# Optimization experiments

Measured on AMD Instinct MI355X. Metric: run time of the kernel, lower is better.

Reference implementation:

```python
import jax, jax.numpy as jnp
import numpy as np

# ---- model constants (match init_kwargs) ----
E = 128; GH = 8; GD = E // GH; GL = 3          # graph emb / heads / layers
SH = 4; SD = E // SH; SL = 4                   # sequence transformer
ATOM = 64; BOND = 16; RBF_K = 32; CUTOFF = 5.0
VOCAB = 64; SEQL = 128
N = 32                                          # nodes per graph (equal-size graphs)
GC = 64; GS = 16; BMOL = 16; DEG = 64; GF = 3   # conf graphs / scaffold graphs / molecules / edges-per-graph
LN_EPS = 1e-5
CENTERS = jnp.linspace(0.0, CUTOFF, RBF_K)
GAMMA = (CUTOFF / (RBF_K - 1)) ** -2            # GaussianRBF gamma = (center spacing)^-2


def _ln(x, g, b):
    mu = x.mean(-1, keepdims=True)
    var = ((x - mu) ** 2).mean(-1, keepdims=True)
    return (x - mu) / jnp.sqrt(var + LN_EPS) * g + b


def _graph_encoder(x, edge_index, edge_attr, pos, G, p):
    # node projection
    h = x @ p["gproj_w"] + p["gproj_b"]                      # [G*N, E]
    # edge features: bond features + RBF(distance)
    d = jnp.clip(edge_attr[:, -1], 0.0, 10.0)
    rbf = jnp.exp(-GAMMA * (d[:, None] - CENTERS) ** 2)       # [M, K]
    ef = jnp.concatenate([edge_attr[:, :-1], rbf], axis=1)    # [M, BOND+K]
    # EdgeNetwork: per-edge matrix (gather -> matvec -> scatter-add)
    M = ef.shape[0]
    m = (ef @ p["elin_w"] + p["elin_b"]).reshape(M, E, E)
    msg = jnp.einsum("mef,mf->me", m, h[edge_index[1]])      # [M, E]
    aggr = jnp.zeros_like(h).at[edge_index[0]].add(msg)
    h = _ln(h + aggr, p["eln_g"], p["eln_b"])
    # dense per-graph layout (equal-size graphs -> reshape, mask is all-true)
    hb = h.reshape(G, N, E)
    pp = pos.reshape(G, N, 3)
    d2 = jnp.sum((pp[:, :, None, :] - pp[:, None, :, :]) ** 2, axis=-1)
    dist = jnp.where(d2 > 0, jnp.sqrt(jnp.where(d2 > 0, d2, 1.0)), 0.0)  # safe cdist
    inv_sqrt_d = 1.0 / np.sqrt(GD)
    for l in range(GL):
        def heads(t):
            return t.reshape(G, N, GH, GD).transpose(0, 2, 1, 3)
        q = heads(hb @ p["gt_qw"][l] + p["gt_qb"][l])
        k = heads(hb @ p["gt_kw"][l] + p["gt_kb"][l])
        v = heads(hb @ p["gt_vw"][l] + p["gt_vb"][l])
        s = jnp.einsum("bhnd,bhmd->bhnm", q, k) * inv_sqrt_d + dist[:, None]
        s = jnp.clip(s, -10.0, 10.0)
        a = jax.nn.softmax(s, axis=-1)                       # all nodes valid -> no mask
        o = jnp.einsum("bhnm,bhmd->bhnd", a, v).transpose(0, 2, 1, 3).reshape(G, N, E)
        o = o @ p["gt_ow"][l] + p["gt_ob"][l]
        x1 = _ln(hb + o, p["gt_ln1g"][l], p["gt_ln1b"][l])
        ff = jax.nn.relu(x1 @ p["gt_f1w"][l] + p["gt_f1b"][l]) @ p["gt_f2w"][l] + p["gt_f2b"][l]
        hb = _ln(x1 + ff, p["gt_ln2g"][l], p["gt_ln2b"][l])
    # masked mean pool with the source's eps in the denominator
    return hb.sum(1) / (N + 1e-8)


def _seq_encoder(tokens, p):
    B, L = tokens.shape
    x = p["tok_emb"][tokens] + p["pos_emb"][:L][None]        # [B, L, E]
    inv_sqrt_d = 1.0 / np.sqrt(SD)
    for l in range(SL):
        qkv = x @ p["se_inw"][l] + p["se_inb"][l]            # [B, L, 3E]
        q, k, v = jnp.split(qkv, 3, axis=-1)
        def heads(t):
            return t.reshape(B, L, SH, SD).transpose(0, 2, 1, 3)
        q, k, v = heads(q), heads(k), heads(v)
        a = jax.nn.softmax(jnp.einsum("bhnd,bhmd->bhnm", q, k) * inv_sqrt_d, axis=-1)
        o = jnp.einsum("bhnm,bhmd->bhnd", a, v).transpose(0, 2, 1, 3).reshape(B, L, E)
        o = o @ p["se_ow"][l] + p["se_ob"][l]
        x = _ln(x + o, p["se_ln1g"][l], p["se_ln1b"][l])      # post-norm (torch default)
        ff = jax.nn.relu(x @ p["se_f1w"][l] + p["se_f1b"][l]) @ p["se_f2w"][l] + p["se_f2b"][l]
        x = _ln(x + ff, p["se_ln2g"][l], p["se_ln2b"][l])
    return x.mean(1)                                          # [B, E]


def _forward(p, conf_edge_index, scaf_edge_index, tokens, conf_per_mol):
    g_all = _graph_encoder(p["conf_x"], conf_edge_index, p["conf_edge_attr"], p["conf_pos"], GC, p)
    conf_emb = g_all.reshape(-1, conf_per_mol, E).mean(1)     # per-molecule conformer mean (equal counts)
    scaf_emb = _graph_encoder(p["scaf_x"], scaf_edge_index, p["scaf_edge_attr"], p["scaf_pos"], GS, p)
    total = conf_emb + scaf_emb
    seq = _seq_encoder(tokens, p)
    # FusionGating
    gate_h = jax.nn.relu(jnp.concatenate([total, seq], -1) @ p["fg1_w"] + p["fg1_b"])
    gate = jax.nn.sigmoid(gate_h @ p["fg2_w"] + p["fg2_b"])
    fused = gate * total + (1.0 - gate) * seq
    # CrossModalAttention: MHA over a length-1 sequence (unsqueeze(0)) -> softmax
    # weights are identically 1, so attn(q_in, kv, kv) == out_proj(v_proj(kv)).
    g, s = fused, fused
    for l in range(2):
        g2s = (s @ p["cm_g2s_vw"][l] + p["cm_g2s_vb"][l]) @ p["cm_g2s_ow"][l] + p["cm_g2s_ob"][l]
        g = _ln(g + g2s, p["cm_n1g"][l], p["cm_n1b"][l])
        s2g = (g @ p["cm_s2g_vw"][l] + p["cm_s2g_vb"][l]) @ p["cm_s2g_ow"][l] + p["cm_s2g_ob"][l]
        s = _ln(s + s2g, p["cm_n2g"][l], p["cm_n2b"][l])
    final = (g + s) * 0.5
    comb = jnp.concatenate([final, p["graph_features"]], -1)
    return (jax.nn.relu(comb @ p["r1_w"] + p["r1_b"]) @ p["r2_w"] + p["r2_b"])[:, 0]


def setup_inputs() -> dict:
    ks = iter(jax.random.split(jax.random.key(0), 64))
    def nrm(shape, s):
        return (jax.random.normal(next(ks), shape) * s).astype(jnp.float32)
    inp = {}
    def mk_graph(prefix, G):
        inp[prefix + "_x"] = nrm((G * N, ATOM), 1.0)
        off = (jnp.arange(G) * N)[:, None]
        src = jax.random.randint(next(ks), (G, DEG), 0, N) + off   # within-graph edges
        dst = jax.random.randint(next(ks), (G, DEG), 0, N) + off
        inp[prefix + "_edge_index"] = jnp.stack([src.ravel(), dst.ravel()]).astype(jnp.int32)
        bond = jax.random.uniform(next(ks), (G * DEG, BOND))
        dist = jax.random.uniform(next(ks), (G * DEG, 1), minval=0.5, maxval=CUTOFF)
        inp[prefix + "_edge_attr"] = jnp.concatenate([bond, dist], 1).astype(jnp.float32)
        inp[prefix + "_pos"] = nrm((G * N, 3), 2.0)
    mk_graph("conf", GC)
    mk_graph("scaf", GS)
    inp["tokens"] = jax.random.randint(next(ks), (BMOL, SEQL), 1, VOCAB).astype(jnp.int32)
    inp["graph_features"] = nrm((BMOL, GF), 1.0)
    inp["conf_per_mol"] = GC // BMOL
    W = 0.05
    inp["gproj_w"] = nrm((ATOM, E), W); inp["gproj_b"] = jnp.zeros(E)
    inp["elin_w"] = nrm((BOND + RBF_K, E * E), W); inp["elin_b"] = jnp.zeros(E * E)
    inp["eln_g"] = jnp.ones(E); inp["eln_b"] = jnp.zeros(E)
    for nm in ["qw", "kw", "vw", "ow"]:
        inp["gt_" + nm] = nrm((GL, E, E), W)
        inp["gt_" + nm[0] + "b"] = jnp.zeros((GL, E))
    inp["gt_ln1g"] = jnp.ones((GL, E)); inp["gt_ln1b"] = jnp.zeros((GL, E))
    inp["gt_f1w"] = nrm((GL, E, 2 * E), W); inp["gt_f1b"] = jnp.zeros((GL, 2 * E))
    inp["gt_f2w"] = nrm((GL, 2 * E, E), W); inp["gt_f2b"] = jnp.zeros((GL, E))
    inp["gt_ln2g"] = jnp.ones((GL, E)); inp["gt_ln2b"] = jnp.zeros((GL, E))
    inp["tok_emb"] = nrm((VOCAB, E), 0.02); inp["pos_emb"] = nrm((256, E), 0.02)
    inp["se_inw"] = nrm((SL, E, 3 * E), W); inp["se_inb"] = jnp.zeros((SL, 3 * E))
    inp["se_ow"] = nrm((SL, E, E), W); inp["se_ob"] = jnp.zeros((SL, E))
    inp["se_ln1g"] = jnp.ones((SL, E)); inp["se_ln1b"] = jnp.zeros((SL, E))
    inp["se_f1w"] = nrm((SL, E, 2 * E), W); inp["se_f1b"] = jnp.zeros((SL, 2 * E))
    inp["se_f2w"] = nrm((SL, 2 * E, E), W); inp["se_f2b"] = jnp.zeros((SL, E))
    inp["se_ln2g"] = jnp.ones((SL, E)); inp["se_ln2b"] = jnp.zeros((SL, E))
    inp["fg1_w"] = nrm((2 * E, 64), W); inp["fg1_b"] = jnp.zeros(64)
    inp["fg2_w"] = nrm((64, E), W); inp["fg2_b"] = jnp.zeros(E)
    for nm in ["g2s", "s2g"]:
        inp["cm_" + nm + "_vw"] = nrm((2, E, E), W); inp["cm_" + nm + "_vb"] = jnp.zeros((2, E))
        inp["cm_" + nm + "_ow"] = nrm((2, E, E), W); inp["cm_" + nm + "_ob"] = jnp.zeros((2, E))
    inp["cm_n1g"] = jnp.ones((2, E)); inp["cm_n1b"] = jnp.zeros((2, E))
    inp["cm_n2g"] = jnp.ones((2, E)); inp["cm_n2b"] = jnp.zeros((2, E))
    inp["r1_w"] = nrm((E + GF, E), W); inp["r1_b"] = jnp.zeros(E)
    inp["r2_w"] = nrm((E, 1), W); inp["r2_b"] = jnp.zeros(1)
    return inp


def reference(conf_x, conf_edge_attr, conf_pos, scaf_x, scaf_edge_attr, scaf_pos, graph_features,
              gproj_w, gproj_b, elin_w, elin_b, eln_g, eln_b,
              gt_qw, gt_qb, gt_kw, gt_kb, gt_vw, gt_vb, gt_ow, gt_ob,
              gt_ln1g, gt_ln1b, gt_f1w, gt_f1b, gt_f2w, gt_f2b, gt_ln2g, gt_ln2b,
              tok_emb, pos_emb,
              se_inw, se_inb, se_ow, se_ob, se_ln1g, se_ln1b, se_f1w, se_f1b, se_f2w, se_f2b, se_ln2g, se_ln2b,
              fg1_w, fg1_b, fg2_w, fg2_b,
              cm_g2s_vw, cm_g2s_vb, cm_g2s_ow, cm_g2s_ob, cm_n1g, cm_n1b,
              cm_s2g_vw, cm_s2g_vb, cm_s2g_ow, cm_s2g_ob, cm_n2g, cm_n2b,
              r1_w, r1_b, r2_w, r2_b,
              conf_edge_index, scaf_edge_index, tokens, conf_per_mol):
    p = dict(locals())
    return _forward(p, conf_edge_index, scaf_edge_index, tokens, conf_per_mol)
```

## Files before the change

### kernel.cpp

```cpp
#include <hip/hip_runtime.h>
#include <hip/hip_bf16.h>


__device__ __forceinline__ float blk_norm(float v, int e, float* sred)
{
  float s = v;
  #pragma unroll
  for (int o = 1; o < 64; o <<= 1) s += __shfl_xor(s, o);
  if ((e & 63) == 0) sred[e >> 6] = s;
  __syncthreads();
  float mean = (sred[0] + sred[1]) * (1.0f / 128.0f);
  __syncthreads();
  float d = v - mean;
  float s2 = d * d;
  #pragma unroll
  for (int o = 1; o < 64; o <<= 1) s2 += __shfl_xor(s2, o);
  if ((e & 63) == 0) sred[e >> 6] = s2;
  __syncthreads();
  float var = (sred[0] + sred[1]) * (1.0f / 128.0f);
  __syncthreads();
  return d / sqrtf(var + 1e-5f);
}

__global__ __launch_bounds__(128) void node_proj_k(
    const float* __restrict__ cx, const float* __restrict__ sx,
    const float* __restrict__ w, const float* __restrict__ b,
    float* __restrict__ h, float* __restrict__ aggr)
{
  int r = blockIdx.x, e = threadIdx.x;
  const float* x = (r < 2048) ? (cx + (size_t)r * 64) : (sx + (size_t)(r - 2048) * 64);
  __shared__ float xs[64];
  if (e < 64) xs[e] = x[e];
  __syncthreads();
  float acc = b[e];
  for (int a = 0; a < 64; a++) acc += xs[a] * w[a * 128 + e];
  h[(size_t)r * 128 + e] = acc;
  aggr[(size_t)r * 128 + e] = 0.0f;
}

__global__ __launch_bounds__(256) void dist_k(
    const float* __restrict__ cpos, const float* __restrict__ spos, float* __restrict__ dist)
{
  int g = blockIdx.x, tid = threadIdx.x;
  __shared__ float P[96];
  const float* p = (g < 64) ? (cpos + (size_t)g * 96) : (spos + (size_t)(g - 64) * 96);
  if (tid < 96) P[tid] = p[tid];
  __syncthreads();
  #pragma unroll
  for (int jj = 0; jj < 4; jj++) {
    int idx = tid * 4 + jj;
    int i = idx >> 5, j = idx & 31;
    float dx = P[i * 3 + 0] - P[j * 3 + 0];
    float dy = P[i * 3 + 1] - P[j * 3 + 1];
    float dz = P[i * 3 + 2] - P[j * 3 + 2];
    float d2 = dx * dx + dy * dy + dz * dz;
    dist[(size_t)g * 1024 + idx] = (d2 > 0.0f) ? sqrtf(d2) : 0.0f;
  }
}

__global__ __launch_bounds__(256) void edge_gemm_k(
    const float* __restrict__ cea, const float* __restrict__ sea,
    const int* __restrict__ cei, const int* __restrict__ sei,
    const float* __restrict__ h,
    const float* __restrict__ elw, const float* __restrict__ elb,
    float* __restrict__ aggr)
{
  __shared__ float efs[32][8];
  __shared__ float As[32][36];
  __shared__ float Bs[32][136];
  const int tid = threadIdx.x;
  const int m0 = blockIdx.x * 32;
  const int kt0 = blockIdx.y * 28;
  const int c0 = kt0 >> 2;
  {
    int t = tid >> 3, cc = tid & 7;
    if (cc < 7) {
      int c = c0 + cc;
      int m = m0 + t;
      const float* attr = (m < 4096) ? (cea + (size_t)m * 17) : (sea + (size_t)(m - 4096) * 17);
      float val;
      if (c < 16) val = attr[c];
      else if (c < 48) {
        float d = fminf(fmaxf(attr[16], 0.0f), 10.0f);
        float t2 = d - (float)((c - 16) * (5.0 / 31.0));
        val = expf(-38.44f * t2 * t2);
      } else val = 1.0f;
      efs[t][cc] = val;
    }
  }
  const int gk = tid & 31, gt = (tid >> 5) * 4;
  float hreg[4][4];
  #pragma unroll
  for (int i = 0; i < 4; i++) {
    int m = m0 + gt + i;
    int dst = (m < 4096) ? cei[4096 + m] : (sei[1024 + (m - 4096)] + 2048);
    const float* hp = h + (size_t)dst * 128 + gk;
    hreg[i][0] = hp[0]; hreg[i][1] = hp[32]; hreg[i][2] = hp[64]; hreg[i][3] = hp[96];
  }
  const int tn = tid & 31, tm = tid >> 5;
  const int e0 = 4 * tn, t0 = 4 * tm;
  const int se = tid >> 1, sk = (tid & 1) * 16;
  float acc[4][4] = {};
  __syncthreads();
  #pragma unroll 1
  for (int kt = kt0; kt < kt0 + 28; kt++) {
    int c = kt >> 2, cc = c - c0, j = kt & 3;
    float4 av;
    av.x = efs[gt + 0][cc] * hreg[0][j];
    av.y = efs[gt + 1][cc] * hreg[1][j];
    av.z = efs[gt + 2][cc] * hreg[2][j];
    av.w = efs[gt + 3][cc] * hreg[3][j];
    *(float4*)&As[gk][gt] = av;
    const float* bp = ((c < 48) ? (elw + (size_t)c * 16384) : elb) + (size_t)se * 128 + j * 32 + sk;
    float4 w0 = *(const float4*)(bp + 0);
    float4 w1 = *(const float4*)(bp + 4);
    float4 w2 = *(const float4*)(bp + 8);
    float4 w3 = *(const float4*)(bp + 12);
    Bs[sk + 0][se] = w0.x;  Bs[sk + 1][se] = w0.y;  Bs[sk + 2][se] = w0.z;  Bs[sk + 3][se] = w0.w;
    Bs[sk + 4][se] = w1.x;  Bs[sk + 5][se] = w1.y;  Bs[sk + 6][se] = w1.z;  Bs[sk + 7][se] = w1.w;
    Bs[sk + 8][se] = w2.x;  Bs[sk + 9][se] = w2.y;  Bs[sk + 10][se] = w2.z; Bs[sk + 11][se] = w2.w;
    Bs[sk + 12][se] = w3.x; Bs[sk + 13][se] = w3.y; Bs[sk + 14][se] = w3.z; Bs[sk + 15][se] = w3.w;
    __syncthreads();
    #pragma unroll
    for (int kk = 0; kk < 32; kk++) {
      float4 a = *(const float4*)&As[kk][t0];
      float4 b = *(const float4*)&Bs[kk][e0];
      acc[0][0] += a.x * b.x; acc[0][1] += a.x * b.y; acc[0][2] += a.x * b.z; acc[0][3] += a.x * b.w;
      acc[1][0] += a.y * b.x; acc[1][1] += a.y * b.y; acc[1][2] += a.y * b.z; acc[1][3] += a.y * b.w;
      acc[2][0] += a.z * b.x; acc[2][1] += a.z * b.y; acc[2][2] += a.z * b.z; acc[2][3] += a.z * b.w;
      acc[3][0] += a.w * b.x; acc[3][1] += a.w * b.y; acc[3][2] += a.w * b.z; acc[3][3] += a.w * b.w;
    }
    __syncthreads();
  }
  #pragma unroll
  for (int i = 0; i < 4; i++) {
    int m = m0 + t0 + i;
    int src = (m < 4096) ? cei[m] : (sei[m - 4096] + 2048);
    float* dst = aggr + (size_t)src * 128 + e0;
    atomicAdd(dst + 0, acc[i][0]);
    atomicAdd(dst + 1, acc[i][1]);
    atomicAdd(dst + 2, acc[i][2]);
    atomicAdd(dst + 3, acc[i][3]);
  }
}

__device__ __forceinline__ void gemm16_body(
    const float* __restrict__ A, const float* __restrict__ Bp,
    const float* __restrict__ biasp, float* __restrict__ Cp,
    int row0, int ldb, int ldc)
{
  __shared__ float Sa[32][20];
  __shared__ float Bs[32][136];
  const int tid = threadIdx.x;
  const int tm = tid >> 5, tn = tid & 31;
  const int t0 = 2 * tm, e0 = 4 * tn;
  const int ar = tid >> 4, ak = (tid & 15) * 2;
  const int bk = tid >> 3, be = (tid & 7) * 16;
  float acc[2][4] = {};
  for (int k0 = 0; k0 < 128; k0 += 32) {
    float2 av = *(const float2*)(A + (size_t)(row0 + ar) * 128 + k0 + ak);
    Sa[ak][ar] = av.x; Sa[ak + 1][ar] = av.y;
    const float* bp = Bp + (size_t)(k0 + bk) * ldb + be;
    float4 b0v = *(const float4*)(bp + 0);
    float4 b1v = *(const float4*)(bp + 4);
    float4 b2v = *(const float4*)(bp + 8);
    float4 b3v = *(const float4*)(bp + 12);
    Bs[bk][be + 0] = b0v.x;  Bs[bk][be + 1] = b0v.y;  Bs[bk][be + 2] = b0v.z;  Bs[bk][be + 3] = b0v.w;
    Bs[bk][be + 4] = b1v.x;  Bs[bk][be + 5] = b1v.y;  Bs[bk][be + 6] = b1v.z;  Bs[bk][be + 7] = b1v.w;
    Bs[bk][be + 8] = b2v.x;  Bs[bk][be + 9] = b2v.y;  Bs[bk][be + 10] = b2v.z; Bs[bk][be + 11] = b2v.w;
    Bs[bk][be + 12] = b3v.x; Bs[bk][be + 13] = b3v.y; Bs[bk][be + 14] = b3v.z; Bs[bk][be + 15] = b3v.w;
    __syncthreads();
    #pragma unroll
    for (int kk = 0; kk < 32; kk++) {
      float2 a = *(const float2*)&Sa[kk][t0];
      float4 b = *(const float4*)&Bs[kk][e0];
      acc[0][0] += a.x * b.x; acc[0][1] += a.x * b.y; acc[0][2] += a.x * b.z; acc[0][3] += a.x * b.w;
      acc[1][0] += a.y * b.x; acc[1][1] += a.y * b.y; acc[1][2] += a.y * b.z; acc[1][3] += a.y * b.w;
    }
    __syncthreads();
  }
  #pragma unroll
  for (int i = 0; i < 2; i++) {
    float* cp = Cp + (size_t)(row0 + t0 + i) * ldc + e0;
    #pragma unroll
    for (int j = 0; j < 4; j++) cp[j] = acc[i][j] + biasp[e0 + j];
  }
}

__global__ __launch_bounds__(256) void qkv_k(
    int gBlocks,
    const float* __restrict__ ghb,
    const float* gqw, const float* gkw, const float* gvw,
    const float* gqb, const float* gkb, const float* gvb, float* gout,
    const float* __restrict__ sxs, const float* sw, const float* sb, float* sout)
{
  int bx = blockIdx.x;
  if (bx < gBlocks) {
    int z = bx / 160, rt = bx % 160;
    const float* B = (z == 0) ? gqw : (z == 1) ? gkw : gvw;
    const float* bias = (z == 0) ? gqb : (z == 1) ? gkb : gvb;
    gemm16_body(ghb, B, bias, gout + (size_t)z * 327680, rt * 16, 128, 128);
  } else {
    int i = bx - gBlocks;
    int z = i >> 7, rt = i & 127;
    gemm16_body(sxs, sw + z * 128, sb + z * 128, sout + z * 128, rt * 16, 384, 384);
  }
}

__device__ __forceinline__ void gattn_body(
    int g, int h, const float* __restrict__ q, const float* __restrict__ k,
    const float* __restrict__ v, const float* __restrict__ dist, float* __restrict__ o)
{
  __shared__ float qs[32][17], ksh[32][17], vsh[32][17], ss[32][33], rs[32];
  const int tid = threadIdx.x;
  {
    int idx = tid * 2;
    int i = idx >> 4, d = idx & 15;
    size_t base = ((size_t)(g * 32 + i)) * 128 + h * 16 + d;
    qs[i][d] = q[base];  qs[i][d + 1] = q[base + 1];
    ksh[i][d] = k[base]; ksh[i][d + 1] = k[base + 1];
    vsh[i][d] = v[base]; vsh[i][d + 1] = v[base + 1];
  }
  __syncthreads();
  {
    int i = tid >> 3, j0 = (tid & 7) * 4;
    for (int j = j0; j < j0 + 4; j++) {
      float a = 0;
      #pragma unroll
      for (int d = 0; d < 16; d++) a += qs[i][d] * ksh[j][d];
      a = a * 0.25f + dist[(size_t)g * 1024 + i * 32 + j];
      ss[i][j] = fminf(fmaxf(a, -10.0f), 10.0f);
    }
  }
  __syncthreads();
  if (tid < 32) {
    float m = -1e30f;
    for (int j = 0; j < 32; j++) m = fmaxf(m, ss[tid][j]);
    float sm = 0;
    for (int j = 0; j < 32; j++) { float ex = expf(ss[tid][j] - m); ss[tid][j] = ex; sm += ex; }
    rs[tid] = 1.0f / sm;
  }
  __syncthreads();
  {
    int idx = tid * 2;
    int i = idx >> 4, d = idx & 15;
    float a0 = 0, a1 = 0;
    for (int j = 0; j < 32; j++) { float wj = ss[i][j]; a0 += wj * vsh[j][d]; a1 += wj * vsh[j][d + 1]; }
    float r = rs[i];
    size_t base = ((size_t)(g * 32 + i)) * 128 + h * 16 + d;
    o[base] = a0 * r; o[base + 1] = a1 * r;
  }
}

__device__ __forceinline__ void sattn_body(
    int b, int h, int qt, const float* __restrict__ qkv, float* __restrict__ o)
{
  __shared__ float ks[128][33];
  __shared__ float vs[128][33];
  __shared__ float qs2[32][33];
  __shared__ float ss2[32][129];
  __shared__ float red[32][8];
  __shared__ float red2[32][8];
  const int tid = threadIdx.x;
  {
    int l = tid >> 1, d0 = (tid & 1) * 16;
    const float* kp = qkv + ((size_t)(b * 128 + l)) * 384 + 128 + h * 32 + d0;
    #pragma unroll
    for (int j = 0; j < 16; j++) { ks[l][d0 + j] = kp[j]; vs[l][d0 + j] = kp[128 + j]; }
  }
  {
    int i = tid >> 3, d0 = (tid & 7) * 4;
    const float* qp = qkv + ((size_t)(b * 128 + qt * 32 + i)) * 384 + h * 32 + d0;
    #pragma unroll
    for (int j = 0; j < 4; j++) qs2[i][d0 + j] = qp[j];
  }
  __syncthreads();
  const int i = tid >> 3, sub = tid & 7;
  {
    int j0 = sub * 16;
    for (int j = j0; j < j0 + 16; j++) {
      float a = 0;
      #pragma unroll
      for (int d = 0; d < 32; d++) a += qs2[i][d] * ks[j][d];
      ss2[i][j] = a * 0.17677669529663687f;
    }
  }
  __syncthreads();
  float m = -1e30f;
  for (int j = sub; j < 128; j += 8) m = fmaxf(m, ss2[i][j]);
  red[i][sub] = m;
  __syncthreads();
  float mm = red[i][0];
  #pragma unroll
  for (int t = 1; t < 8; t++) mm = fmaxf(mm, red[i][t]);
  float ps = 0;
  for (int j = sub; j < 128; j += 8) { float ex = expf(ss2[i][j] - mm); ss2[i][j] = ex; ps += ex; }
  red2[i][sub] = ps;
  __syncthreads();
  float sm = 0;
  #pragma unroll
  for (int t = 0; t < 8; t++) sm += red2[i][t];
  float rinv = 1.0f / sm;
  {
    int d0 = sub * 4;
    float a0 = 0, a1 = 0, a2 = 0, a3 = 0;
    for (int j = 0; j < 128; j++) {
      float wj = ss2[i][j];
      a0 += wj * vs[j][d0 + 0]; a1 += wj * vs[j][d0 + 1];
      a2 += wj * vs[j][d0 + 2]; a3 += wj * vs[j][d0 + 3];
    }
    float* op = o + ((size_t)(b * 128 + qt * 32 + i)) * 128 + h * 32 + d0;
    op[0] = a0 * rinv; op[1] = a1 * rinv; op[2] = a2 * rinv; op[3] = a3 * rinv;
  }
}

__global__ __launch_bounds__(256) void attn_k(
    int gBlocks, const float* q, const float* k, const float* v,
    const float* dist, float* go, const float* qkv, float* so)
{
  int bx = blockIdx.x;
  if (bx < gBlocks) gattn_body(bx >> 3, bx & 7, q, k, v, dist, go);
  else { int i = bx - gBlocks; sattn_body(i >> 4, (i >> 2) & 3, i & 3, qkv, so); }
}

__device__ __forceinline__ void tail_body(
    int row0, const float* __restrict__ A,
    const float* __restrict__ Wo, const float* __restrict__ bo, const float* __restrict__ res,
    const float* __restrict__ g1, const float* __restrict__ b1n,
    const float* __restrict__ W1, const float* __restrict__ b1f,
    const float* __restrict__ W2, const float* __restrict__ b2f,
    const float* __restrict__ g2, const float* __restrict__ b2n,
    float* __restrict__ Out)
{
  __shared__ float x1[16][132];
  __shared__ float hid[16][260];
  __shared__ __align__(16) float sbuf[4352];
  __shared__ float Sa[32][20];
  float (*BsA)[136] = (float(*)[136])sbuf;
  float (*Bs1)[260] = (float(*)[260])sbuf;
  float (*Bs2)[136] = (float(*)[136])sbuf;
  const int tid = threadIdx.x;
  {
    const int tm = tid >> 5, tn = tid & 31;
    const int t0 = 2 * tm, e0 = 4 * tn;
    const int ar = tid >> 4, ak = (tid & 15) * 2;
    const int bk = tid >> 3, be = (tid & 7) * 16;
    float acc[2][4] = {};
    for (int k0 = 0; k0 < 128; k0 += 32) {
      float2 av = *(const float2*)(A + (size_t)(row0 + ar) * 128 + k0 + ak);
      Sa[ak][ar] = av.x; Sa[ak + 1][ar] = av.y;
      const float* bp = Wo + (size_t)(k0 + bk) * 128 + be;
      float4 b0v = *(const float4*)(bp + 0);
      float4 b1v = *(const float4*)(bp + 4);
      float4 b2v = *(const float4*)(bp + 8);
      float4 b3v = *(const float4*)(bp + 12);
      BsA[bk][be + 0] = b0v.x;  BsA[bk][be + 1] = b0v.y;  BsA[bk][be + 2] = b0v.z;  BsA[bk][be + 3] = b0v.w;
      BsA[bk][be + 4] = b1v.x;  BsA[bk][be + 5] = b1v.y;  BsA[bk][be + 6] = b1v.z;  BsA[bk][be + 7] = b1v.w;
      BsA[bk][be + 8] = b2v.x;  BsA[bk][be + 9] = b2v.y;  BsA[bk][be + 10] = b2v.z; BsA[bk][be + 11] = b2v.w;
      BsA[bk][be + 12] = b3v.x; BsA[bk][be + 13] = b3v.y; BsA[bk][be + 14] = b3v.z; BsA[bk][be + 15] = b3v.w;
      __syncthreads();
      #pragma unroll
      for (int kk = 0; kk < 32; kk++) {
        float2 a = *(const float2*)&Sa[kk][t0];
        float4 b = *(const float4*)&BsA[kk][e0];
        acc[0][0] += a.x * b.x; acc[0][1] += a.x * b.y; acc[0][2] += a.x * b.z; acc[0][3] += a.x * b.w;
        acc[1][0] += a.y * b.x; acc[1][1] += a.y * b.y; acc[1][2] += a.y * b.z; acc[1][3] += a.y * b.w;
      }
      __syncthreads();
    }
    #pragma unroll
    for (int i = 0; i < 2; i++) {
      int r = row0 + t0 + i;
      float v0 = acc[i][0] + bo[e0 + 0] + res[(size_t)r * 128 + e0 + 0];
      float v1 = acc[i][1] + bo[e0 + 1] + res[(size_t)r * 128 + e0 + 1];
      float v2 = acc[i][2] + bo[e0 + 2] + res[(size_t)r * 128 + e0 + 2];
      float v3 = acc[i][3] + bo[e0 + 3] + res[(size_t)r * 128 + e0 + 3];
      float s = v0 + v1 + v2 + v3;
      #pragma unroll
      for (int o = 1; o < 32; o <<= 1) s += __shfl_xor(s, o);
      float mean = s * (1.0f / 128.0f);
      float d0 = v0 - mean, d1 = v1 - mean, d2 = v2 - mean, d3 = v3 - mean;
      float sq = d0 * d0 + d1 * d1 + d2 * d2 + d3 * d3;
      #pragma unroll
      for (int o = 1; o < 32; o <<= 1) sq += __shfl_xor(sq, o);
      float rstd = 1.0f / sqrtf(sq * (1.0f / 128.0f) + 1e-5f);
      x1[t0 + i][e0 + 0] = d0 * rstd * g1[e0 + 0] + b1n[e0 + 0];
      x1[t0 + i][e0 + 1] = d1 * rstd * g1[e0 + 1] + b1n[e0 + 1];
      x1[t0 + i][e0 + 2] = d2 * rstd * g1[e0 + 2] + b1n[e0 + 2];
      x1[t0 + i][e0 + 3] = d3 * rstd * g1[e0 + 3] + b1n[e0 + 3];
    }
  }
  __syncthreads();
  {
    const int tm = tid >> 6, tn = tid & 63;
    const int t0 = 4 * tm, e0 = 4 * tn;
    const int ar = tid >> 4, ak = tid & 15;
    const int bk = tid >> 4, be = (tid & 15) * 16;
    float acc[4][4] = {};
    for (int k0 = 0; k0 < 128; k0 += 16) {
      Sa[ak][ar] = x1[ar][k0 + ak];
      const float* bp = W1 + (size_t)(k0 + bk) * 256 + be;
      float4 b0v = *(const float4*)(bp + 0);
      float4 b1v = *(const float4*)(bp + 4);
      float4 b2v = *(const float4*)(bp + 8);
      float4 b3v = *(const float4*)(bp + 12);
      Bs1[bk][be + 0] = b0v.x;  Bs1[bk][be + 1] = b0v.y;  Bs1[bk][be + 2] = b0v.z;  Bs1[bk][be + 3] = b0v.w;
      Bs1[bk][be + 4] = b1v.x;  Bs1[bk][be + 5] = b1v.y;  Bs1[bk][be + 6] = b1v.z;  Bs1[bk][be + 7] = b1v.w;
      Bs1[bk][be + 8] = b2v.x;  Bs1[bk][be + 9] = b2v.y;  Bs1[bk][be + 10] = b2v.z; Bs1[bk][be + 11] = b2v.w;
      Bs1[bk][be + 12] = b3v.x; Bs1[bk][be + 13] = b3v.y; Bs1[bk][be + 14] = b3v.z; Bs1[bk][be + 15] = b3v.w;
      __syncthreads();
      #pragma unroll
      for (int kk = 0; kk < 16; kk++) {
        float4 a = *(const float4*)&Sa[kk][t0];
        float4 b = *(const float4*)&Bs1[kk][e0];
        acc[0][0] += a.x * b.x; acc[0][1] += a.x * b.y; acc[0][2] += a.x * b.z; acc[0][3] += a.x * b.w;
        acc[1][0] += a.y * b.x; acc[1][1] += a.y * b.y; acc[1][2] += a.y * b.z; acc[1][3] += a.y * b.w;
        acc[2][0] += a.z * b.x; acc[2][1] += a.z * b.y; acc[2][2] += a.z * b.z; acc[2][3] += a.z * b.w;
        acc[3][0] += a.w * b.x; acc[3][1] += a.w * b.y; acc[3][2] += a.w * b.z; acc[3][3] += a.w * b.w;
      }
      __syncthreads();
    }
    #pragma unroll
    for (int i = 0; i < 4; i++) {
      float4 hv;
      hv.x = fmaxf(acc[i][0] + b1f[e0 + 0], 0.0f);
      hv.y = fmaxf(acc[i][1] + b1f[e0 + 1], 0.0f);
      hv.z = fmaxf(acc[i][2] + b1f[e0 + 2], 0.0f);
      hv.w = fmaxf(acc[i][3] + b1f[e0 + 3], 0.0f);
      *(float4*)&hid[t0 + i][e0] = hv;
    }
  }
  __syncthreads();
  {
    const int tm = tid >> 5, tn = tid & 31;
    const int t0 = 2 * tm, e0 = 4 * tn;
    const int bk = tid >> 3, be = (tid & 7) * 16;
    float acc[2][4] = {};
    for (int k0 = 0; k0 < 256; k0 += 32) {
      const float* bp = W2 + (size_t)(k0 + bk) * 128 + be;
      float4 b0v = *(const float4*)(bp + 0);
      float4 b1v = *(const float4*)(bp + 4);
      float4 b2v = *(const float4*)(bp + 8);
      float4 b3v = *(const float4*)(bp + 12);
      Bs2[bk][be + 0] = b0v.x;  Bs2[bk][be + 1] = b0v.y;  Bs2[bk][be + 2] = b0v.z;  Bs2[bk][be + 3] = b0v.w;
      Bs2[bk][be + 4] = b1v.x;  Bs2[bk][be + 5] = b1v.y;  Bs2[bk][be + 6] = b1v.z;  Bs2[bk][be + 7] = b1v.w;
      Bs2[bk][be + 8] = b2v.x;  Bs2[bk][be + 9] = b2v.y;  Bs2[bk][be + 10] = b2v.z; Bs2[bk][be + 11] = b2v.w;
      Bs2[bk][be + 12] = b3v.x; Bs2[bk][be + 13] = b3v.y; Bs2[bk][be + 14] = b3v.z; Bs2[bk][be + 15] = b3v.w;
      __syncthreads();
      #pragma unroll
      for (int kk = 0; kk < 32; kk++) {
        float a0 = hid[t0 + 0][k0 + kk];
        float a1 = hid[t0 + 1][k0 + kk];
        float4 b = *(const float4*)&Bs2[kk][e0];
        acc[0][0] += a0 * b.x; acc[0][1] += a0 * b.y; acc[0][2] += a0 * b.z; acc[0][3] += a0 * b.w;
        acc[1][0] += a1 * b.x; acc[1][1] += a1 * b.y; acc[1][2] += a1 * b.z; acc[1][3] += a1 * b.w;
      }
      __syncthreads();
    }
    #pragma unroll
    for (int i = 0; i < 2; i++) {
      int r = row0 + t0 + i;
      float v0 = acc[i][0] + b2f[e0 + 0] + x1[t0 + i][e0 + 0];
      float v1 = acc[i][1] + b2f[e0 + 1] + x1[t0 + i][e0 + 1];
      float v2 = acc[i][2] + b2f[e0 + 2] + x1[t0 + i][e0 + 2];
      float v3 = acc[i][3] + b2f[e0 + 3] + x1[t0 + i][e0 + 3];
      float s = v0 + v1 + v2 + v3;
      #pragma unroll
      for (int o = 1; o < 32; o <<= 1) s += __shfl_xor(s, o);
      float mean = s * (1.0f / 128.0f);
      float d0 = v0 - mean, d1 = v1 - mean, d2 = v2 - mean, d3 = v3 - mean;
      float sq = d0 * d0 + d1 * d1 + d2 * d2 + d3 * d3;
      #pragma unroll
      for (int o = 1; o < 32; o <<= 1) sq += __shfl_xor(sq, o);
      float rstd = 1.0f / sqrtf(sq * (1.0f / 128.0f) + 1e-5f);
      float* cp = Out + (size_t)r * 128 + e0;
      cp[0] = d0 * rstd * g2[e0 + 0] + b2n[e0 + 0];
      cp[1] = d1 * rstd * g2[e0 + 1] + b2n[e0 + 1];
      cp[2] = d2 * rstd * g2[e0 + 2] + b2n[e0 + 2];
      cp[3] = d3 * rstd * g2[e0 + 3] + b2n[e0 + 3];
    }
  }
}

__global__ __launch_bounds__(256) void tail_k(
    int gBlocks,
    const float* gA, const float* gWo, const float* gbo, const float* gres,
    const float* gg1, const float* gb1, const float* gW1, const float* gbf1,
    const float* gW2, const float* gbf2, const float* gg2, const float* gb2, float* gOut,
    const float* sA, const float* sWo, const float* sbo, const float* sres,
    const float* sg1, const float* sb1, const float* sW1, const float* sbf1,
    const float* sW2, const float* sbf2, const float* sg2, const float* sb2, float* sOut)
{
  int bx = blockIdx.x;
  if (bx < gBlocks)
    tail_body(bx * 16, gA, gWo, gbo, gres, gg1, gb1, gW1, gbf1, gW2, gbf2, gg2, gb2, gOut);
  else
    tail_body((bx - gBlocks) * 16, sA, sWo, sbo, sres, sg1, sb1, sW1, sbf1, sW2, sbf2, sg2, sb2, sOut);
}

__global__ __launch_bounds__(128) void ln_k(
    const float* __restrict__ x, const float* __restrict__ res,
    const float* __restrict__ g, const float* __restrict__ b, float* __restrict__ out)
{
  __shared__ float sred[2];
  int r = blockIdx.x, e = threadIdx.x;
  size_t idx = (size_t)r * 128 + e;
  float v = x[idx] + res[idx];
  float nv = blk_norm(v, e, sred);
  out[idx] = nv * g[e] + b[e];
}

__global__ __launch_bounds__(128) void embed_k(
    const int* __restrict__ tokens, const float* __restrict__ tok_emb,
    const float* __restrict__ pos_emb, float* __restrict__ xs)
{
  int r = blockIdx.x, e = threadIdx.x;
  int tk = tokens[r];
  xs[(size_t)r * 128 + e] = tok_emb[(size_t)tk * 128 + e] + pos_emb[(size_t)(r & 127) * 128 + e];
}

__global__ __launch_bounds__(128) void head_k(
    const float* __restrict__ hb, const float* __restrict__ xs, const float* __restrict__ gfeat,
    const float* fg1w, const float* fg1b, const float* fg2w, const float* fg2b,
    const float* g2s_vw, const float* g2s_vb, const float* g2s_ow, const float* g2s_ob,
    const float* n1g, const float* n1b,
    const float* s2g_vw, const float* s2g_vb, const float* s2g_ow, const float* s2g_ob,
    const float* n2g, const float* n2b,
    const float* r1w, const float* r1b, const float* r2w, const float* r2b,
    float* __restrict__ out)
{
  __shared__ float T[128], S[128], G[128], Sm[128], t1[128], t2[128], gh[64], sred[2];
  int mol = blockIdx.x, e = threadIdx.x;
  {
    float cs = 0;
    for (int c = 0; c < 4; c++) {
      int g = mol * 4 + c;
      float s = 0;
      for (int i = 0; i < 32; i++) s += hb[((size_t)(g * 32 + i)) * 128 + e];
      cs += s * (1.0f / 32.0f);
    }
    cs *= 0.25f;
    float s2 = 0;
    int g = 64 + mol;
    for (int i = 0; i < 32; i++) s2 += hb[((size_t)(g * 32 + i)) * 128 + e];
    T[e] = cs + s2 * (1.0f / 32.0f);
    float ss = 0;
    for (int l = 0; l < 128; l++) ss += xs[((size_t)(mol * 128 + l)) * 128 + e];
    S[e] = ss * (1.0f / 128.0f);
  }
  __syncthreads();
  if (e < 64) {
    float a = fg1b[e];
    for (int f = 0; f < 128; f++) a += T[f] * fg1w[f * 64 + e];
    for (int f = 0; f < 128; f++) a += S[f] * fg1w[(128 + f) * 64 + e];
    gh[e] = fmaxf(a, 0.0f);
  }
  __syncthreads();
  {
    float a = fg2b[e];
    for (int j = 0; j < 64; j++) a += gh[j] * fg2w[j * 128 + e];
    float gate = 1.0f / (1.0f + expf(-a));
    float fu = gate * T[e] + (1.0f - gate) * S[e];
    G[e] = fu; Sm[e] = fu;
  }
  __syncthreads();
  for (int l = 0; l < 2; l++) {
    const float* vw = g2s_vw + (size_t)l * 16384; const float* vb = g2s_vb + l * 128;
    const float* ow = g2s_ow + (size_t)l * 16384; const float* ob = g2s_ob + l * 128;
    float a = vb[e];
    for (int f = 0; f < 128; f++) a += Sm[f] * vw[f * 128 + e];
    t1[e] = a;
    __syncthreads();
    a = ob[e];
    for (int f = 0; f < 128; f++) a += t1[f] * ow[f * 128 + e];
    float nv = blk_norm(G[e] + a, e, sred);
    G[e] = nv * n1g[l * 128 + e] + n1b[l * 128 + e];
    __syncthreads();
    const float* vw2 = s2g_vw + (size_t)l * 16384; const float* vb2 = s2g_vb + l * 128;
    const float* ow2 = s2g_ow + (size_t)l * 16384; const float* ob2 = s2g_ob + l * 128;
    a = vb2[e];
    for (int f = 0; f < 128; f++) a += G[f] * vw2[f * 128 + e];
    t1[e] = a;
    __syncthreads();
    a = ob2[e];
    for (int f = 0; f < 128; f++) a += t1[f] * ow2[f * 128 + e];
    nv = blk_norm(Sm[e] + a, e, sred);
    Sm[e] = nv * n2g[l * 128 + e] + n2b[l * 128 + e];
    __syncthreads();
  }
  t2[e] = 0.5f * (G[e] + Sm[e]);
  __syncthreads();
  float a = r1b[e];
  for (int f = 0; f < 128; f++) a += t2[f] * r1w[f * 128 + e];
  for (int f = 0; f < 3; f++) a += gfeat[mol * 3 + f] * r1w[(128 + f) * 128 + e];
  a = fmaxf(a, 0.0f);
  float p = a * r2w[e];
  #pragma unroll
  for (int o = 1; o < 64; o <<= 1) p += __shfl_xor(p, o);
  if ((e & 63) == 0) sred[e >> 6] = p;
  __syncthreads();
  if (e == 0) out[mol] = sred[0] + sred[1] + r2b[0];
}

extern "C" void kernel_launch(void* const* d_in, const int* in_sizes, int n_in,
                              void* d_out, int out_size, void* d_ws, size_t ws_size,
                              hipStream_t stream)
{
  (void)n_in; (void)out_size; (void)ws_size;
  const bool dict = (in_sizes[1] == 8192);
  auto IN = [&](int di, int si) { return d_in[dict ? di : si]; };

  const float* conf_x   = (const float*)IN(0, 0);
  const int*   conf_ei  = (const int*)  IN(1, 63);
  const float* conf_ea  = (const float*)IN(2, 1);
  const float* conf_pos = (const float*)IN(3, 2);
  const float* scaf_x   = (const float*)IN(4, 3);
  const int*   scaf_ei  = (const int*)  IN(5, 64);
  const float* scaf_ea  = (const float*)IN(6, 4);
  const float* scaf_pos = (const float*)IN(7, 5);
  const int*   tokens   = (const int*)  IN(8, 65);
  const float* gfeat    = (const float*)IN(9, 6);
  const float* gproj_w  = (const float*)IN(11, 7);
  const float* gproj_b  = (const float*)IN(12, 8);
  const float* elin_w   = (const float*)IN(13, 9);
  const float* elin_b   = (const float*)IN(14, 10);
  const float* eln_g    = (const float*)IN(15, 11);
  const float* eln_b    = (const float*)IN(16, 12);
  const float* gt_qw    = (const float*)IN(17, 13);
  const float* gt_qb    = (const float*)IN(18, 14);
  const float* gt_kw    = (const float*)IN(19, 15);
  const float* gt_kb    = (const float*)IN(20, 16);
  const float* gt_vw    = (const float*)IN(21, 17);
  const float* gt_vb    = (const float*)IN(22, 18);
  const float* gt_ow    = (const float*)IN(23, 19);
  const float* gt_ob    = (const float*)IN(24, 20);
  const float* gt_ln1g  = (const float*)IN(25, 21);
  const float* gt_ln1b  = (const float*)IN(26, 22);
  const float* gt_f1w   = (const float*)IN(27, 23);
  const float* gt_f1b   = (const float*)IN(28, 24);
  const float* gt_f2w   = (const float*)IN(29, 25);
  const float* gt_f2b   = (const float*)IN(30, 26);
  const float* gt_ln2g  = (const float*)IN(31, 27);
  const float* gt_ln2b  = (const float*)IN(32, 28);
  const float* tok_emb  = (const float*)IN(33, 29);
  const float* pos_emb  = (const float*)IN(34, 30);
  const float* se_inw   = (const float*)IN(35, 31);
  const float* se_inb   = (const float*)IN(36, 32);
  const float* se_ow    = (const float*)IN(37, 33);
  const float* se_ob    = (const float*)IN(38, 34);
  const float* se_ln1g  = (const float*)IN(39, 35);
  const float* se_ln1b  = (const float*)IN(40, 36);
  const float* se_f1w   = (const float*)IN(41, 37);
  const float* se_f1b   = (const float*)IN(42, 38);
  const float* se_f2w   = (const float*)IN(43, 39);
  const float* se_f2b   = (const float*)IN(44, 40);
  const float* se_ln2g  = (const float*)IN(45, 41);
  const float* se_ln2b  = (const float*)IN(46, 42);
  const float* fg1_w    = (const float*)IN(47, 43);
  const float* fg1_b    = (const float*)IN(48, 44);
  const float* fg2_w    = (const float*)IN(49, 45);
  const float* fg2_b    = (const float*)IN(50, 46);
  const float* cm_g2s_vw = (const float*)IN(51, 47);
  const float* cm_g2s_vb = (const float*)IN(52, 48);
  const float* cm_g2s_ow = (const float*)IN(53, 49);
  const float* cm_g2s_ob = (const float*)IN(54, 50);
  const float* cm_s2g_vw = (const float*)IN(55, 53);
  const float* cm_s2g_vb = (const float*)IN(56, 54);
  const float* cm_s2g_ow = (const float*)IN(57, 55);
  const float* cm_s2g_ob = (const float*)IN(58, 56);
  const float* cm_n1g   = (const float*)IN(59, 51);
  const float* cm_n1b   = (const float*)IN(60, 52);
  const float* cm_n2g   = (const float*)IN(61, 57);
  const float* cm_n2b   = (const float*)IN(62, 58);
  const float* r1_w     = (const float*)IN(63, 59);
  const float* r1_b     = (const float*)IN(64, 60);
  const float* r2_w     = (const float*)IN(65, 61);
  const float* r2_b     = (const float*)IN(66, 62);
  float* out = (float*)d_out;

  float* w = (float*)d_ws;
  size_t off = 0;
  auto alloc = [&](size_t n) { float* p = w + off; off += n; return p; };
  float* h     = alloc(2560 * 128);
  float* aggr  = alloc(2560 * 128);
  float* hb    = alloc(2560 * 128);
  float* distb = alloc(80 * 1024);
  float* qb    = alloc(3 * 327680);
  float* atto  = alloc(327680);
  float* xs2   = alloc(2048 * 128);
  float* qkv3  = alloc(2048 * 384);
  float* satto = alloc(2048 * 128);
  float* xsfin = alloc(2048 * 128);

  node_proj_k<<<2560, 128, 0, stream>>>(conf_x, scaf_x, gproj_w, gproj_b, h, aggr);
  dist_k<<<80, 256, 0, stream>>>(conf_pos, scaf_pos, distb);
  edge_gemm_k<<<dim3(160, 7), 256, 0, stream>>>(conf_ea, scaf_ea, conf_ei, scaf_ei, h, elin_w, elin_b, aggr);
  ln_k<<<2560, 128, 0, stream>>>(aggr, h, eln_g, eln_b, hb);
  embed_k<<<2048, 128, 0, stream>>>(tokens, tok_emb, pos_emb, xs2);

  for (int l = 0; l < 4; l++) {
    const bool hasG = (l < 3);
    const int lg = hasG ? l : 0;
    const int gq = hasG ? 480 : 0;
    const int ga = hasG ? 640 : 0;
    const int gt = hasG ? 160 : 0;
    float* sOut = (l == 3) ? xsfin : xs2;
    qkv_k<<<gq + 384, 256, 0, stream>>>(gq,
        hb, gt_qw + (size_t)lg * 16384, gt_kw + (size_t)lg * 16384, gt_vw + (size_t)lg * 16384,
        gt_qb + lg * 128, gt_kb + lg * 128, gt_vb + lg * 128, qb,
        xs2, se_inw + (size_t)l * 49152, se_inb + l * 384, qkv3);
    attn_k<<<ga + 256, 256, 0, stream>>>(ga, qb, qb + 327680, qb + 655360, distb, atto, qkv3, satto);
    tail_k<<<gt + 128, 256, 0, stream>>>(gt,
        atto, gt_ow + (size_t)lg * 16384, gt_ob + lg * 128, hb,
        gt_ln1g + lg * 128, gt_ln1b + lg * 128,
        gt_f1w + (size_t)lg * 32768, gt_f1b + lg * 256,
        gt_f2w + (size_t)lg * 32768, gt_f2b + lg * 128,
        gt_ln2g + lg * 128, gt_ln2b + lg * 128, hb,
        satto, se_ow + (size_t)l * 16384, se_ob + l * 128, xs2,
        se_ln1g + l * 128, se_ln1b + l * 128,
        se_f1w + (size_t)l * 32768, se_f1b + l * 256,
        se_f2w + (size_t)l * 32768, se_f2b + l * 128,
        se_ln2g + l * 128, se_ln2b + l * 128, sOut);
  }

  head_k<<<16, 128, 0, stream>>>(hb, xsfin, gfeat,
                                 fg1_w, fg1_b, fg2_w, fg2_b,
                                 cm_g2s_vw, cm_g2s_vb, cm_g2s_ow, cm_g2s_ob, cm_n1g, cm_n1b,
                                 cm_s2g_vw, cm_s2g_vb, cm_s2g_ow, cm_s2g_ob, cm_n2g, cm_n2b,
                                 r1_w, r1_b, r2_w, r2_b, out);
}
```

Before: 663.6 us.

## Fuse front kernels and restructure small GEMMs to stage A in LDS

Node projection, distance and embedding kernels are merged into one launch to cut launch overhead. The QKV and tail GEMMs now stage the whole 16x128 A tile in shared memory and read B directly from global memory per column, dropping the K-tiled B staging and most barriers. Sequence attention streams K and V in 32-row chunks through a shared buffer, and shared memory is unioned to cut LDS footprint and raise occupancy. The cost is uncached-in-LDS global reads of the weights per block and more barriers in attention.

```diff
diff --git a/kernel.cpp b/kernel.cpp
--- a/kernel.cpp
+++ b/kernel.cpp
@@ -22,39 +22,45 @@
   return d / sqrtf(var + 1e-5f);
 }
 
-__global__ __launch_bounds__(128) void node_proj_k(
+__global__ __launch_bounds__(256) void front_k(
     const float* __restrict__ cx, const float* __restrict__ sx,
     const float* __restrict__ w, const float* __restrict__ b,
-    float* __restrict__ h, float* __restrict__ aggr)
-{
-  int r = blockIdx.x, e = threadIdx.x;
-  const float* x = (r < 2048) ? (cx + (size_t)r * 64) : (sx + (size_t)(r - 2048) * 64);
-  __shared__ float xs[64];
-  if (e < 64) xs[e] = x[e];
-  __syncthreads();
-  float acc = b[e];
-  for (int a = 0; a < 64; a++) acc += xs[a] * w[a * 128 + e];
-  h[(size_t)r * 128 + e] = acc;
-  aggr[(size_t)r * 128 + e] = 0.0f;
-}
-
-__global__ __launch_bounds__(256) void dist_k(
-    const float* __restrict__ cpos, const float* __restrict__ spos, float* __restrict__ dist)
-{
-  int g = blockIdx.x, tid = threadIdx.x;
-  __shared__ float P[96];
-  const float* p = (g < 64) ? (cpos + (size_t)g * 96) : (spos + (size_t)(g - 64) * 96);
-  if (tid < 96) P[tid] = p[tid];
-  __syncthreads();
-  #pragma unroll
-  for (int jj = 0; jj < 4; jj++) {
-    int idx = tid * 4 + jj;
-    int i = idx >> 5, j = idx & 31;
-    float dx = P[i * 3 + 0] - P[j * 3 + 0];
-    float dy = P[i * 3 + 1] - P[j * 3 + 1];
-    float dz = P[i * 3 + 2] - P[j * 3 + 2];
-    float d2 = dx * dx + dy * dy + dz * dz;
-    dist[(size_t)g * 1024 + idx] = (d2 > 0.0f) ? sqrtf(d2) : 0.0f;
+    float* __restrict__ h, float* __restrict__ aggr,
+    const float* __restrict__ cpos, const float* __restrict__ spos, float* __restrict__ dist,
+    const int* __restrict__ tokens, const float* __restrict__ tok_emb,
+    const float* __restrict__ pos_emb, float* __restrict__ xs)
+{
+  __shared__ float sP[128];
+  const int bx = blockIdx.x, tid = threadIdx.x;
+  if (bx < 1280) {
+    int r = bx * 2 + (tid >> 7), e = tid & 127;
+    const float* x = (r < 2048) ? (cx + (size_t)r * 64) : (sx + (size_t)(r - 2048) * 64);
+    float* xrow = sP + (tid >> 7) * 64;
+    if (e < 64) xrow[e] = x[e];
+    __syncthreads();
+    float acc = b[e];
+    for (int a = 0; a < 64; a++) acc += xrow[a] * w[a * 128 + e];
+    h[(size_t)r * 128 + e] = acc;
+    aggr[(size_t)r * 128 + e] = 0.0f;
+  } else if (bx < 1360) {
+    int g = bx - 1280;
+    const float* p = (g < 64) ? (cpos + (size_t)g * 96) : (spos + (size_t)(g - 64) * 96);
+    if (tid < 96) sP[tid] = p[tid];
+    __syncthreads();
+    #pragma unroll
+    for (int jj = 0; jj < 4; jj++) {
+      int idx = tid * 4 + jj;
+      int i = idx >> 5, j = idx & 31;
+      float dx = sP[i * 3 + 0] - sP[j * 3 + 0];
+      float dy = sP[i * 3 + 1] - sP[j * 3 + 1];
+      float dz = sP[i * 3 + 2] - sP[j * 3 + 2];
+      float d2 = dx * dx + dy * dy + dz * dz;
+      dist[(size_t)g * 1024 + idx] = (d2 > 0.0f) ? sqrtf(d2) : 0.0f;
+    }
+  } else {
+    int r = (bx - 1360) * 2 + (tid >> 7), e = tid & 127;
+    int tk = tokens[r];
+    xs[(size_t)r * 128 + e] = tok_emb[(size_t)tk * 128 + e] + pos_emb[(size_t)(r & 127) * 128 + e];
   }
 }
 
@@ -144,47 +150,36 @@
   }
 }
 
-__device__ __forceinline__ void gemm16_body(
+__device__ __forceinline__ void sgemm16_body(float (*Al)[132],
     const float* __restrict__ A, const float* __restrict__ Bp,
     const float* __restrict__ biasp, float* __restrict__ Cp,
     int row0, int ldb, int ldc)
 {
-  __shared__ float Sa[32][20];
-  __shared__ float Bs[32][136];
   const int tid = threadIdx.x;
-  const int tm = tid >> 5, tn = tid & 31;
-  const int t0 = 2 * tm, e0 = 4 * tn;
-  const int ar = tid >> 4, ak = (tid & 15) * 2;
-  const int bk = tid >> 3, be = (tid & 7) * 16;
-  float acc[2][4] = {};
-  for (int k0 = 0; k0 < 128; k0 += 32) {
-    float2 av = *(const float2*)(A + (size_t)(row0 + ar) * 128 + k0 + ak);
-    Sa[ak][ar] = av.x; Sa[ak + 1][ar] = av.y;
-    const float* bp = Bp + (size_t)(k0 + bk) * ldb + be;
-    float4 b0v = *(const float4*)(bp + 0);
-    float4 b1v = *(const float4*)(bp + 4);
-    float4 b2v = *(const float4*)(bp + 8);
-    float4 b3v = *(const float4*)(bp + 12);
-    Bs[bk][be + 0] = b0v.x;  Bs[bk][be + 1] = b0v.y;  Bs[bk][be + 2] = b0v.z;  Bs[bk][be + 3] = b0v.w;
-    Bs[bk][be + 4] = b1v.x;  Bs[bk][be + 5] = b1v.y;  Bs[bk][be + 6] = b1v.z;  Bs[bk][be + 7] = b1v.w;
-    Bs[bk][be + 8] = b2v.x;  Bs[bk][be + 9] = b2v.y;  Bs[bk][be + 10] = b2v.z; Bs[bk][be + 11] = b2v.w;
-    Bs[bk][be + 12] = b3v.x; Bs[bk][be + 13] = b3v.y; Bs[bk][be + 14] = b3v.z; Bs[bk][be + 15] = b3v.w;
-    __syncthreads();
-    #pragma unroll
-    for (int kk = 0; kk < 32; kk++) {
-      float2 a = *(const float2*)&Sa[kk][t0];
-      float4 b = *(const float4*)&Bs[kk][e0];
-      acc[0][0] += a.x * b.x; acc[0][1] += a.x * b.y; acc[0][2] += a.x * b.z; acc[0][3] += a.x * b.w;
-      acc[1][0] += a.y * b.x; acc[1][1] += a.y * b.y; acc[1][2] += a.y * b.z; acc[1][3] += a.y * b.w;
-    }
-    __syncthreads();
-  }
-  #pragma unroll
-  for (int i = 0; i < 2; i++) {
-    float* cp = Cp + (size_t)(row0 + t0 + i) * ldc + e0;
-    #pragma unroll
-    for (int j = 0; j < 4; j++) cp[j] = acc[i][j] + biasp[e0 + j];
-  }
+  const int c = tid & 127, rg = tid >> 7;
+  for (int i = tid; i < 512; i += 256) {
+    int r = i >> 5, k4 = (i & 31) << 2;
+    *(float4*)&Al[r][k4] = *(const float4*)(A + (size_t)(row0 + r) * 128 + k4);
+  }
+  __syncthreads();
+  float acc[8] = {};
+  const float* bp = Bp + c;
+  #pragma unroll 4
+  for (int k = 0; k < 128; k += 4) {
+    float b0 = bp[(size_t)(k + 0) * ldb];
+    float b1 = bp[(size_t)(k + 1) * ldb];
+    float b2 = bp[(size_t)(k + 2) * ldb];
+    float b3 = bp[(size_t)(k + 3) * ldb];
+    #pragma unroll
+    for (int i = 0; i < 8; i++) {
+      float4 a = *(const float4*)&Al[rg * 8 + i][k];
+      acc[i] += a.x * b0; acc[i] += a.y * b1; acc[i] += a.z * b2; acc[i] += a.w * b3;
+    }
+  }
+  float bia = biasp[c];
+  #pragma unroll
+  for (int i = 0; i < 8; i++)
+    Cp[(size_t)(row0 + rg * 8 + i) * ldc + c] = acc[i] + bia;
 }
 
 __global__ __launch_bounds__(256) void qkv_k(
@@ -194,32 +189,33 @@
     const float* gqb, const float* gkb, const float* gvb, float* gout,
     const float* __restrict__ sxs, const float* sw, const float* sb, float* sout)
 {
+  __shared__ float Al[16][132];
   int bx = blockIdx.x;
   if (bx < gBlocks) {
     int z = bx / 160, rt = bx % 160;
     const float* B = (z == 0) ? gqw : (z == 1) ? gkw : gvw;
     const float* bias = (z == 0) ? gqb : (z == 1) ? gkb : gvb;
-    gemm16_body(ghb, B, bias, gout + (size_t)z * 327680, rt * 16, 128, 128);
+    sgemm16_body(Al, ghb, B, bias, gout + (size_t)z * 327680, rt * 16, 128, 128);
   } else {
     int i = bx - gBlocks;
     int z = i >> 7, rt = i & 127;
-    gemm16_body(sxs, sw + z * 128, sb + z * 128, sout + z * 128, rt * 16, 384, 384);
-  }
-}
-
-__device__ __forceinline__ void gattn_body(
-    int g, int h, const float* __restrict__ q, const float* __restrict__ k,
+    sgemm16_body(Al, sxs, sw + z * 128, sb + z * 128, sout + z * 128, rt * 16, 384, 384);
+  }
+}
+
+struct __align__(16) GAttnSm { float qs[32][17], ksh[32][17], vsh[32][17], ss[32][33], rs[32]; };
+__device__ __forceinline__ void gattn_body(GAttnSm& sm, int g, int h,
+    const float* __restrict__ q, const float* __restrict__ k,
     const float* __restrict__ v, const float* __restrict__ dist, float* __restrict__ o)
 {
-  __shared__ float qs[32][17], ksh[32][17], vsh[32][17], ss[32][33], rs[32];
   const int tid = threadIdx.x;
   {
     int idx = tid * 2;
     int i = idx >> 4, d = idx & 15;
     size_t base = ((size_t)(g * 32 + i)) * 128 + h * 16 + d;
-    qs[i][d] = q[base];  qs[i][d + 1] = q[base + 1];
-    ksh[i][d] = k[base]; ksh[i][d + 1] = k[base + 1];
-    vsh[i][d] = v[base]; vsh[i][d + 1] = v[base + 1];
+    sm.qs[i][d] = q[base];  sm.qs[i][d + 1] = q[base + 1];
+    sm.ksh[i][d] = k[base]; sm.ksh[i][d + 1] = k[base + 1];
+    sm.vsh[i][d] = v[base]; sm.vsh[i][d + 1] = v[base + 1];
   }
   __syncthreads();
   {
@@ -227,104 +223,114 @@
     for (int j = j0; j < j0 + 4; j++) {
       float a = 0;
       #pragma unroll
-      for (int d = 0; d < 16; d++) a += qs[i][d] * ksh[j][d];
+      for (int d = 0; d < 16; d++) a += sm.qs[i][d] * sm.ksh[j][d];
       a = a * 0.25f + dist[(size_t)g * 1024 + i * 32 + j];
-      ss[i][j] = fminf(fmaxf(a, -10.0f), 10.0f);
+      sm.ss[i][j] = fminf(fmaxf(a, -10.0f), 10.0f);
     }
   }
   __syncthreads();
   if (tid < 32) {
     float m = -1e30f;
-    for (int j = 0; j < 32; j++) m = fmaxf(m, ss[tid][j]);
-    float sm = 0;
-    for (int j = 0; j < 32; j++) { float ex = expf(ss[tid][j] - m); ss[tid][j] = ex; sm += ex; }
-    rs[tid] = 1.0f / sm;
+    for (int j = 0; j < 32; j++) m = fmaxf(m, sm.ss[tid][j]);
+    float s = 0;
+    for (int j = 0; j < 32; j++) { float ex = expf(sm.ss[tid][j] - m); sm.ss[tid][j] = ex; s += ex; }
+    sm.rs[tid] = 1.0f / s;
   }
   __syncthreads();
   {
     int idx = tid * 2;
     int i = idx >> 4, d = idx & 15;
     float a0 = 0, a1 = 0;
-    for (int j = 0; j < 32; j++) { float wj = ss[i][j]; a0 += wj * vsh[j][d]; a1 += wj * vsh[j][d + 1]; }
-    float r = rs[i];
+    for (int j = 0; j < 32; j++) { float wj = sm.ss[i][j]; a0 += wj * sm.vsh[j][d]; a1 += wj * sm.vsh[j][d + 1]; }
+    float r = sm.rs[i];
     size_t base = ((size_t)(g * 32 + i)) * 128 + h * 16 + d;
     o[base] = a0 * r; o[base + 1] = a1 * r;
   }
 }
 
-__device__ __forceinline__ void sattn_body(
-    int b, int h, int qt, const float* __restrict__ qkv, float* __restrict__ o)
-{
-  __shared__ float ks[128][33];
-  __shared__ float vs[128][33];
-  __shared__ float qs2[32][33];
-  __shared__ float ss2[32][129];
-  __shared__ float red[32][8];
-  __shared__ float red2[32][8];
+struct __align__(16) SAttnSm { float kv[32][33], qs2[32][33], ss2[32][129], red[32][8], red2[32][8]; };
+__device__ __forceinline__ void sattn_body(SAttnSm& sm, int b, int h, int qt,
+    const float* __restrict__ qkv, float* __restrict__ o)
+{
   const int tid = threadIdx.x;
-  {
-    int l = tid >> 1, d0 = (tid & 1) * 16;
-    const float* kp = qkv + ((size_t)(b * 128 + l)) * 384 + 128 + h * 32 + d0;
-    #pragma unroll
-    for (int j = 0; j < 16; j++) { ks[l][d0 + j] = kp[j]; vs[l][d0 + j] = kp[128 + j]; }
-  }
   {
     int i = tid >> 3, d0 = (tid & 7) * 4;
     const float* qp = qkv + ((size_t)(b * 128 + qt * 32 + i)) * 384 + h * 32 + d0;
-    #pragma unroll
-    for (int j = 0; j < 4; j++) qs2[i][d0 + j] = qp[j];
-  }
-  __syncthreads();
+    sm.qs2[i][d0 + 0] = qp[0]; sm.qs2[i][d0 + 1] = qp[1];
+    sm.qs2[i][d0 + 2] = qp[2]; sm.qs2[i][d0 + 3] = qp[3];
+  }
   const int i = tid >> 3, sub = tid & 7;
-  {
-    int j0 = sub * 16;
-    for (int j = j0; j < j0 + 16; j++) {
-      float a = 0;
-      #pragma unroll
-      for (int d = 0; d < 32; d++) a += qs2[i][d] * ks[j][d];
-      ss2[i][j] = a * 0.17677669529663687f;
-    }
-  }
-  __syncthreads();
+  for (int jt = 0; jt < 4; jt++) {
+    {
+      int r = tid >> 3, dd = (tid & 7) * 4;
+      const float* kp = qkv + ((size_t)(b * 128 + jt * 32 + r)) * 384 + 128 + h * 32 + dd;
+      float4 kv4 = *(const float4*)kp;
+      sm.kv[r][dd + 0] = kv4.x; sm.kv[r][dd + 1] = kv4.y;
+      sm.kv[r][dd + 2] = kv4.z; sm.kv[r][dd + 3] = kv4.w;
+    }
+    __syncthreads();
+    {
+      int j0 = jt * 32 + sub * 4;
+      for (int j = j0; j < j0 + 4; j++) {
+        int jr = j - jt * 32;
+        float a = 0;
+        #pragma unroll
+        for (int d = 0; d < 32; d++) a += sm.qs2[i][d] * sm.kv[jr][d];
+        sm.ss2[i][j] = a * 0.17677669529663687f;
+      }
+    }
+    __syncthreads();
+  }
   float m = -1e30f;
-  for (int j = sub; j < 128; j += 8) m = fmaxf(m, ss2[i][j]);
-  red[i][sub] = m;
-  __syncthreads();
-  float mm = red[i][0];
-  #pragma unroll
-  for (int t = 1; t < 8; t++) mm = fmaxf(mm, red[i][t]);
+  for (int j = sub; j < 128; j += 8) m = fmaxf(m, sm.ss2[i][j]);
+  sm.red[i][sub] = m;
+  __syncthreads();
+  float mm = sm.red[i][0];
+  #pragma unroll
+  for (int t = 1; t < 8; t++) mm = fmaxf(mm, sm.red[i][t]);
   float ps = 0;
-  for (int j = sub; j < 128; j += 8) { float ex = expf(ss2[i][j] - mm); ss2[i][j] = ex; ps += ex; }
-  red2[i][sub] = ps;
-  __syncthreads();
-  float sm = 0;
-  #pragma unroll
-  for (int t = 0; t < 8; t++) sm += red2[i][t];
-  float rinv = 1.0f / sm;
-  {
-    int d0 = sub * 4;
-    float a0 = 0, a1 = 0, a2 = 0, a3 = 0;
-    for (int j = 0; j < 128; j++) {
-      float wj = ss2[i][j];
-      a0 += wj * vs[j][d0 + 0]; a1 += wj * vs[j][d0 + 1];
-      a2 += wj * vs[j][d0 + 2]; a3 += wj * vs[j][d0 + 3];
-    }
-    float* op = o + ((size_t)(b * 128 + qt * 32 + i)) * 128 + h * 32 + d0;
-    op[0] = a0 * rinv; op[1] = a1 * rinv; op[2] = a2 * rinv; op[3] = a3 * rinv;
-  }
-}
-
+  for (int j = sub; j < 128; j += 8) { float ex = expf(sm.ss2[i][j] - mm); sm.ss2[i][j] = ex; ps += ex; }
+  sm.red2[i][sub] = ps;
+  __syncthreads();
+  float s = 0;
+  #pragma unroll
+  for (int t = 0; t < 8; t++) s += sm.red2[i][t];
+  float rinv = 1.0f / s;
+  float a0 = 0, a1 = 0, a2 = 0, a3 = 0;
+  const int d0 = sub * 4;
+  for (int jt = 0; jt < 4; jt++) {
+    __syncthreads();
+    {
+      int r = tid >> 3, dd = (tid & 7) * 4;
+      const float* vp = qkv + ((size_t)(b * 128 + jt * 32 + r)) * 384 + 256 + h * 32 + dd;
+      float4 vv = *(const float4*)vp;
+      sm.kv[r][dd + 0] = vv.x; sm.kv[r][dd + 1] = vv.y;
+      sm.kv[r][dd + 2] = vv.z; sm.kv[r][dd + 3] = vv.w;
+    }
+    __syncthreads();
+    for (int jr = 0; jr < 32; jr++) {
+      float wj = sm.ss2[i][jt * 32 + jr];
+      a0 += wj * sm.kv[jr][d0 + 0]; a1 += wj * sm.kv[jr][d0 + 1];
+      a2 += wj * sm.kv[jr][d0 + 2]; a3 += wj * sm.kv[jr][d0 + 3];
+    }
+  }
+  float* op = o + ((size_t)(b * 128 + qt * 32 + i)) * 128 + h * 32 + d0;
+  op[0] = a0 * rinv; op[1] = a1 * rinv; op[2] = a2 * rinv; op[3] = a3 * rinv;
+}
+
+union AttnU { GAttnSm a; SAttnSm s; };
 __global__ __launch_bounds__(256) void attn_k(
     int gBlocks, const float* q, const float* k, const float* v,
     const float* dist, float* go, const float* qkv, float* so)
 {
+  __shared__ AttnU u;
   int bx = blockIdx.x;
-  if (bx < gBlocks) gattn_body(bx >> 3, bx & 7, q, k, v, dist, go);
-  else { int i = bx - gBlocks; sattn_body(i >> 4, (i >> 2) & 3, i & 3, qkv, so); }
-}
-
-__device__ __forceinline__ void tail_body(
-    int row0, const float* __restrict__ A,
+  if (bx < gBlocks) gattn_body(u.a, bx >> 3, bx & 7, q, k, v, dist, go);
+  else { int i = bx - gBlocks; sattn_body(u.s, i >> 4, (i >> 2) & 3, i & 3, qkv, so); }
+}
+
+struct __align__(16) TailSm2 { float x1v[16][132]; float big[16][260]; };
+__device__ __forceinline__ void tail_body(TailSm2& sm, int row0, const float* __restrict__ A,
     const float* __restrict__ Wo, const float* __restrict__ bo, const float* __restrict__ res,
     const float* __restrict__ g1, const float* __restrict__ b1n,
     const float* __restrict__ W1, const float* __restrict__ b1f,
@@ -332,49 +338,42 @@
     const float* __restrict__ g2, const float* __restrict__ b2n,
     float* __restrict__ Out)
 {
-  __shared__ float x1[16][132];
-  __shared__ float hid[16][260];
-  __shared__ __align__(16) float sbuf[4352];
-  __shared__ float Sa[32][20];
-  float (*BsA)[136] = (float(*)[136])sbuf;
-  float (*Bs1)[260] = (float(*)[260])sbuf;
-  float (*Bs2)[136] = (float(*)[136])sbuf;
   const int tid = threadIdx.x;
+  const int c = tid & 127, rg = tid >> 7;
+  for (int i = tid; i < 512; i += 256) {
+    int r = i >> 5, k4 = (i & 31) << 2;
+    *(float4*)&sm.big[r][k4] = *(const float4*)(A + (size_t)(row0 + r) * 128 + k4);
+  }
+  __syncthreads();
+  {
+    float acc[8] = {};
+    const float* bp = Wo + c;
+    #pragma unroll 4
+    for (int k = 0; k < 128; k += 4) {
+      float b0 = bp[(k + 0) * 128], b1 = bp[(k + 1) * 128];
+      float b2 = bp[(k + 2) * 128], b3 = bp[(k + 3) * 128];
+      #pragma unroll
+      for (int i = 0; i < 8; i++) {
+        float4 a = *(const float4*)&sm.big[rg * 8 + i][k];
+        acc[i] += a.x * b0; acc[i] += a.y * b1; acc[i] += a.z * b2; acc[i] += a.w * b3;
+      }
+    }
+    float bia = bo[c];
+    #pragma unroll
+    for (int i = 0; i < 8; i++) {
+      int r = rg * 8 + i;
+      sm.x1v[r][c] = acc[i] + bia + res[(size_t)(row0 + r) * 128 + c];
+    }
+  }
+  __syncthreads();
   {
     const int tm = tid >> 5, tn = tid & 31;
     const int t0 = 2 * tm, e0 = 4 * tn;
-    const int ar = tid >> 4, ak = (tid & 15) * 2;
-    const int bk = tid >> 3, be = (tid & 7) * 16;
-    float acc[2][4] = {};
-    for (int k0 = 0; k0 < 128; k0 += 32) {
-      float2 av = *(const float2*)(A + (size_t)(row0 + ar) * 128 + k0 + ak);
-      Sa[ak][ar] = av.x; Sa[ak + 1][ar] = av.y;
-      const float* bp = Wo + (size_t)(k0 + bk) * 128 + be;
-      float4 b0v = *(const float4*)(bp + 0);
-      float4 b1v = *(const float4*)(bp + 4);
-      float4 b2v = *(const float4*)(bp + 8);
-      float4 b3v = *(const float4*)(bp + 12);
-      BsA[bk][be + 0] = b0v.x;  BsA[bk][be + 1] = b0v.y;  BsA[bk][be + 2] = b0v.z;  BsA[bk][be + 3] = b0v.w;
-      BsA[bk][be + 4] = b1v.x;  BsA[bk][be + 5] = b1v.y;  BsA[bk][be + 6] = b1v.z;  BsA[bk][be + 7] = b1v.w;
-      BsA[bk][be + 8] = b2v.x;  BsA[bk][be + 9] = b2v.y;  BsA[bk][be + 10] = b2v.z; BsA[bk][be + 11] = b2v.w;
-      BsA[bk][be + 12] = b3v.x; BsA[bk][be + 13] = b3v.y; BsA[bk][be + 14] = b3v.z; BsA[bk][be + 15] = b3v.w;
-      __syncthreads();
-      #pragma unroll
-      for (int kk = 0; kk < 32; kk++) {
-        float2 a = *(const float2*)&Sa[kk][t0];
-        float4 b = *(const float4*)&BsA[kk][e0];
-        acc[0][0] += a.x * b.x; acc[0][1] += a.x * b.y; acc[0][2] += a.x * b.z; acc[0][3] += a.x * b.w;
-        acc[1][0] += a.y * b.x; acc[1][1] += a.y * b.y; acc[1][2] += a.y * b.z; acc[1][3] += a.y * b.w;
-      }
-      __syncthreads();
-    }
     #pragma unroll
     for (int i = 0; i < 2; i++) {
-      int r = row0 + t0 + i;
-      float v0 = acc[i][0] + bo[e0 + 0] + res[(size_t)r * 128 + e0 + 0];
-      float v1 = acc[i][1] + bo[e0 + 1] + res[(size_t)r * 128 + e0 + 1];
-      float v2 = acc[i][2] + bo[e0 + 2] + res[(size_t)r * 128 + e0 + 2];
-      float v3 = acc[i][3] + bo[e0 + 3] + res[(size_t)r * 128 + e0 + 3];
+      int r = t0 + i;
+      float v0 = sm.x1v[r][e0 + 0], v1 = sm.x1v[r][e0 + 1];
+      float v2 = sm.x1v[r][e0 + 2], v3 = sm.x1v[r][e0 + 3];
       float s = v0 + v1 + v2 + v3;
       #pragma unroll
       for (int o = 1; o < 32; o <<= 1) s += __shfl_xor(s, o);
@@ -384,86 +383,63 @@
       #pragma unroll
       for (int o = 1; o < 32; o <<= 1) sq += __shfl_xor(sq, o);
       float rstd = 1.0f / sqrtf(sq * (1.0f / 128.0f) + 1e-5f);
-      x1[t0 + i][e0 + 0] = d0 * rstd * g1[e0 + 0] + b1n[e0 + 0];
-      x1[t0 + i][e0 + 1] = d1 * rstd * g1[e0 + 1] + b1n[e0 + 1];
-      x1[t0 + i][e0 + 2] = d2 * rstd * g1[e0 + 2] + b1n[e0 + 2];
-      x1[t0 + i][e0 + 3] = d3 * rstd * g1[e0 + 3] + b1n[e0 + 3];
-    }
-  }
-  __syncthreads();
-  {
-    const int tm = tid >> 6, tn = tid & 63;
-    const int t0 = 4 * tm, e0 = 4 * tn;
-    const int ar = tid >> 4, ak = tid & 15;
-    const int bk = tid >> 4, be = (tid & 15) * 16;
-    float acc[4][4] = {};
-    for (int k0 = 0; k0 < 128; k0 += 16) {
-      Sa[ak][ar] = x1[ar][k0 + ak];
-      const float* bp = W1 + (size_t)(k0 + bk) * 256 + be;
-      float4 b0v = *(const float4*)(bp + 0);
-      float4 b1v = *(const float4*)(bp + 4);
-      float4 b2v = *(const float4*)(bp + 8);
-      float4 b3v = *(const float4*)(bp + 12);
-      Bs1[bk][be + 0] = b0v.x;  Bs1[bk][be + 1] = b0v.y;  Bs1[bk][be + 2] = b0v.z;  Bs1[bk][be + 3] = b0v.w;
-      Bs1[bk][be + 4] = b1v.x;  Bs1[bk][be + 5] = b1v.y;  Bs1[bk][be + 6] = b1v.z;  Bs1[bk][be + 7] = b1v.w;
-      Bs1[bk][be + 8] = b2v.x;  Bs1[bk][be + 9] = b2v.y;  Bs1[bk][be + 10] = b2v.z; Bs1[bk][be + 11] = b2v.w;
-      Bs1[bk][be + 12] = b3v.x; Bs1[bk][be + 13] = b3v.y; Bs1[bk][be + 14] = b3v.z; Bs1[bk][be + 15] = b3v.w;
-      __syncthreads();
-      #pragma unroll
-      for (int kk = 0; kk < 16; kk++) {
-        float4 a = *(const float4*)&Sa[kk][t0];
-        float4 b = *(const float4*)&Bs1[kk][e0];
-        acc[0][0] += a.x * b.x; acc[0][1] += a.x * b.y; acc[0][2] += a.x * b.z; acc[0][3] += a.x * b.w;
-        acc[1][0] += a.y * b.x; acc[1][1] += a.y * b.y; acc[1][2] += a.y * b.z; acc[1][3] += a.y * b.w;
-        acc[2][0] += a.z * b.x; acc[2][1] += a.z * b.y; acc[2][2] += a.z * b.z; acc[2][3] += a.z * b.w;
-        acc[3][0] += a.w * b.x; acc[3][1] += a.w * b.y; acc[3][2] += a.w * b.z; acc[3][3] += a.w * b.w;
+      sm.x1v[r][e0 + 0] = d0 * rstd * g1[e0 + 0] + b1n[e0 + 0];
+      sm.x1v[r][e0 + 1] = d1 * rstd * g1[e0 + 1] + b1n[e0 + 1];
+      sm.x1v[r][e0 + 2] = d2 * rstd * g1[e0 + 2] + b1n[e0 + 2];
+      sm.x1v[r][e0 + 3] = d3 * rstd * g1[e0 + 3] + b1n[e0 + 3];
+    }
+  }
+  __syncthreads();
+  {
+    float acc[16] = {};
+    const float* bp = W1 + tid;
+    #pragma unroll 2
+    for (int k = 0; k < 128; k += 4) {
+      float b0 = bp[(k + 0) * 256], b1 = bp[(k + 1) * 256];
+      float b2 = bp[(k + 2) * 256], b3 = bp[(k + 3) * 256];
+      #pragma unroll
+      for (int i = 0; i < 16; i++) {
+        float4 a = *(const float4*)&sm.x1v[i][k];
+        acc[i] += a.x * b0; acc[i] += a.y * b1; acc[i] += a.z * b2; acc[i] += a.w * b3;
       }
-      __syncthreads();
-    }
-    #pragma unroll
-    for (int i = 0; i < 4; i++) {
-      float4 hv;
-      hv.x = fmaxf(acc[i][0] + b1f[e0 + 0], 0.0f);
-      hv.y = fmaxf(acc[i][1] + b1f[e0 + 1], 0.0f);
-      hv.z = fmaxf(acc[i][2] + b1f[e0 + 2], 0.0f);
-      hv.w = fmaxf(acc[i][3] + b1f[e0 + 3], 0.0f);
-      *(float4*)&hid[t0 + i][e0] = hv;
-    }
+    }
+    float bia = b1f[tid];
+    __syncthreads();
+    #pragma unroll
+    for (int i = 0; i < 16; i++)
+      sm.big[i][tid] = fmaxf(acc[i] + bia, 0.0f);
+  }
+  __syncthreads();
+  {
+    float acc[8] = {};
+    const float* bp = W2 + c;
+    #pragma unroll 4
+    for (int k = 0; k < 256; k += 4) {
+      float b0 = bp[(k + 0) * 128], b1 = bp[(k + 1) * 128];
+      float b2 = bp[(k + 2) * 128], b3 = bp[(k + 3) * 128];
+      #pragma unroll
+      for (int i = 0; i < 8; i++) {
+        float4 a = *(const float4*)&sm.big[rg * 8 + i][k];
+        acc[i] += a.x * b0; acc[i] += a.y * b1; acc[i] += a.z * b2; acc[i] += a.w * b3;
+      }
+    }
+    float bia = b2f[c];
+    float v[8];
+    #pragma unroll
+    for (int i = 0; i < 8; i++) v[i] = acc[i] + bia + sm.x1v[rg * 8 + i][c];
+    __syncthreads();
+    #pragma unroll
+    for (int i = 0; i < 8; i++) sm.x1v[rg * 8 + i][c] = v[i];
   }
   __syncthreads();
   {
     const int tm = tid >> 5, tn = tid & 31;
     const int t0 = 2 * tm, e0 = 4 * tn;
-    const int bk = tid >> 3, be = (tid & 7) * 16;
-    float acc[2][4] = {};
-    for (int k0 = 0; k0 < 256; k0 += 32) {
-      const float* bp = W2 + (size_t)(k0 + bk) * 128 + be;
-      float4 b0v = *(const float4*)(bp + 0);
-      float4 b1v = *(const float4*)(bp + 4);
-      float4 b2v = *(const float4*)(bp + 8);
-      float4 b3v = *(const float4*)(bp + 12);
-      Bs2[bk][be + 0] = b0v.x;  Bs2[bk][be + 1] = b0v.y;  Bs2[bk][be + 2] = b0v.z;  Bs2[bk][be + 3] = b0v.w;
-      Bs2[bk][be + 4] = b1v.x;  Bs2[bk][be + 5] = b1v.y;  Bs2[bk][be + 6] = b1v.z;  Bs2[bk][be + 7] = b1v.w;
-      Bs2[bk][be + 8] = b2v.x;  Bs2[bk][be + 9] = b2v.y;  Bs2[bk][be + 10] = b2v.z; Bs2[bk][be + 11] = b2v.w;
-      Bs2[bk][be + 12] = b3v.x; Bs2[bk][be + 13] = b3v.y; Bs2[bk][be + 14] = b3v.z; Bs2[bk][be + 15] = b3v.w;
-      __syncthreads();
-      #pragma unroll
-      for (int kk = 0; kk < 32; kk++) {
-        float a0 = hid[t0 + 0][k0 + kk];
-        float a1 = hid[t0 + 1][k0 + kk];
-        float4 b = *(const float4*)&Bs2[kk][e0];
-        acc[0][0] += a0 * b.x; acc[0][1] += a0 * b.y; acc[0][2] += a0 * b.z; acc[0][3] += a0 * b.w;
-        acc[1][0] += a1 * b.x; acc[1][1] += a1 * b.y; acc[1][2] += a1 * b.z; acc[1][3] += a1 * b.w;
-      }
-      __syncthreads();
-    }
     #pragma unroll
     for (int i = 0; i < 2; i++) {
-      int r = row0 + t0 + i;
-      float v0 = acc[i][0] + b2f[e0 + 0] + x1[t0 + i][e0 + 0];
-      float v1 = acc[i][1] + b2f[e0 + 1] + x1[t0 + i][e0 + 1];
-      float v2 = acc[i][2] + b2f[e0 + 2] + x1[t0 + i][e0 + 2];
-      float v3 = acc[i][3] + b2f[e0 + 3] + x1[t0 + i][e0 + 3];
+      int r = t0 + i;
+      float v0 = sm.x1v[r][e0 + 0], v1 = sm.x1v[r][e0 + 1];
+      float v2 = sm.x1v[r][e0 + 2], v3 = sm.x1v[r][e0 + 3];
       float s = v0 + v1 + v2 + v3;
       #pragma unroll
       for (int o = 1; o < 32; o <<= 1) s += __shfl_xor(s, o);
@@ -473,7 +449,7 @@
       #pragma unroll
       for (int o = 1; o < 32; o <<= 1) sq += __shfl_xor(sq, o);
       float rstd = 1.0f / sqrtf(sq * (1.0f / 128.0f) + 1e-5f);
-      float* cp = Out + (size_t)r * 128 + e0;
+      float* cp = Out + (size_t)(row0 + r) * 128 + e0;
       cp[0] = d0 * rstd * g2[e0 + 0] + b2n[e0 + 0];
       cp[1] = d1 * rstd * g2[e0 + 1] + b2n[e0 + 1];
       cp[2] = d2 * rstd * g2[e0 + 2] + b2n[e0 + 2];
@@ -491,11 +467,12 @@
     const float* sg1, const float* sb1, const float* sW1, const float* sbf1,
     const float* sW2, const float* sbf2, const float* sg2, const float* sb2, float* sOut)
 {
+  __shared__ TailSm2 sm;
   int bx = blockIdx.x;
   if (bx < gBlocks)
-    tail_body(bx * 16, gA, gWo, gbo, gres, gg1, gb1, gW1, gbf1, gW2, gbf2, gg2, gb2, gOut);
+    tail_body(sm, bx * 16, gA, gWo, gbo, gres, gg1, gb1, gW1, gbf1, gW2, gbf2, gg2, gb2, gOut);
   else
-    tail_body((bx - gBlocks) * 16, sA, sWo, sbo, sres, sg1, sb1, sW1, sbf1, sW2, sbf2, sg2, sb2, sOut);
+    tail_body(sm, (bx - gBlocks) * 16, sA, sWo, sbo, sres, sg1, sb1, sW1, sbf1, sW2, sbf2, sg2, sb2, sOut);
 }
 
 __global__ __launch_bounds__(128) void ln_k(
@@ -508,15 +485,6 @@
   float v = x[idx] + res[idx];
   float nv = blk_norm(v, e, sred);
   out[idx] = nv * g[e] + b[e];
-}
-
-__global__ __launch_bounds__(128) void embed_k(
-    const int* __restrict__ tokens, const float* __restrict__ tok_emb,
-    const float* __restrict__ pos_emb, float* __restrict__ xs)
-{
-  int r = blockIdx.x, e = threadIdx.x;
-  int tk = tokens[r];
-  xs[(size_t)r * 128 + e] = tok_emb[(size_t)tk * 128 + e] + pos_emb[(size_t)(r & 127) * 128 + e];
 }
 
 __global__ __launch_bounds__(128) void head_k(
@@ -692,11 +660,11 @@
   float* satto = alloc(2048 * 128);
   float* xsfin = alloc(2048 * 128);
 
-  node_proj_k<<<2560, 128, 0, stream>>>(conf_x, scaf_x, gproj_w, gproj_b, h, aggr);
-  dist_k<<<80, 256, 0, stream>>>(conf_pos, scaf_pos, distb);
+  front_k<<<2384, 256, 0, stream>>>(conf_x, scaf_x, gproj_w, gproj_b, h, aggr,
+                                    conf_pos, scaf_pos, distb,
+                                    tokens, tok_emb, pos_emb, xs2);
   edge_gemm_k<<<dim3(160, 7), 256, 0, stream>>>(conf_ea, scaf_ea, conf_ei, scaf_ei, h, elin_w, elin_b, aggr);
   ln_k<<<2560, 128, 0, stream>>>(aggr, h, eln_g, eln_b, hb);
-  embed_k<<<2048, 128, 0, stream>>>(tokens, tok_emb, pos_emb, xs2);
 
   for (int l = 0; l < 4; l++) {
     const bool hasG = (l < 3);
```

Result: slower. 757.4 us (+14.1%).
